# Performance work log

Hardware: AMD Instinct MI355X
Metric: run time of the kernel (lower is better)

## Reference

```python
import jax, jax.numpy as jnp
import numpy as np

N_, C_, H_, W_ = 8, 256, 64, 64
HEADS = 8
KS = 3
K2 = KS * KS
OUT = 256
HD = OUT // HEADS
STRIDE = 1
PAD = 1


def setup_inputs() -> dict:
    key = jax.random.key(0)
    ks = jax.random.split(key, 8)
    s = 0.05
    return {
        "input_features": jax.random.normal(ks[0], (N_, C_, H_, W_), jnp.float32),
        "Wq": jax.random.normal(ks[1], (OUT, C_), jnp.float32) * s,
        "Wk": jax.random.normal(ks[2], (OUT, C_), jnp.float32) * s,
        "Wv": jax.random.normal(ks[3], (OUT, C_), jnp.float32) * s,
        "off_w": jax.random.normal(ks[4], (HEADS * K2 * 2, C_, KS, KS), jnp.float32) * 0.01,
        "off_b": jnp.zeros((HEADS * K2 * 2,), jnp.float32),
        "attn_w": jax.random.normal(ks[5], (HEADS * K2, C_, KS, KS), jnp.float32) * 0.01,
        "attn_b": jnp.zeros((HEADS * K2,), jnp.float32),
        "Wo": jax.random.normal(ks[6], (OUT, OUT), jnp.float32) * s,
    }


def _conv2d(x, w, b):
    out = jax.lax.conv_general_dilated(
        x, w, (STRIDE, STRIDE), [(PAD, PAD), (PAD, PAD)],
        dimension_numbers=("NCHW", "OIHW", "NCHW"))
    return out + b[None, :, None, None]


def reference(input_features, Wq, Wk, Wv, off_w, off_b, attn_w, attn_b, Wo):
    x = input_features
    N, C, H, W = x.shape
    # query/key are projected but never used downstream in the original module
    q = jnp.einsum("oc,nchw->nohw", Wq, x)
    k = jnp.einsum("oc,nchw->nohw", Wk, x)
    v = jnp.einsum("oc,nchw->nohw", Wv, x)  # [N, OUT, H, W]

    offsets = _conv2d(x, off_w, off_b)                       # [N, HEADS*K2*2, Ho, Wo]
    aw = jax.nn.sigmoid(_conv2d(x, attn_w, attn_b))          # [N, HEADS*K2, Ho, Wo]
    Ho, Wo_sp = offsets.shape[2], offsets.shape[3]

    gx_base = jnp.linspace(-1.0, 1.0, Wo_sp)
    gy_base = jnp.linspace(-1.0, 1.0, Ho)

    # per-head, per-point (x,y) offsets, scaled by 2/[W,H] as in the source
    off = offsets.reshape(N, HEADS, K2, 2, Ho, Wo_sp)
    gx = gx_base[None, None, None, None, :] + off[:, :, :, 0] * (2.0 / W)  # [N,H,K2,Ho,Wo]
    gy = gy_base[None, None, None, :, None] + off[:, :, :, 1] * (2.0 / H)

    # grid_sample bilinear, align_corners=True, padding_mode='zeros'
    xp = (gx + 1.0) * 0.5 * (W - 1)
    yp = (gy + 1.0) * 0.5 * (H - 1)
    x0 = jnp.floor(xp).astype(jnp.int32)
    y0 = jnp.floor(yp).astype(jnp.int32)
    x1 = x0 + 1
    y1 = y0 + 1
    wx1 = xp - x0
    wx0 = 1.0 - wx1
    wy1 = yp - y0
    wy0 = 1.0 - wy1

    vf = v.reshape(N, HEADS, HD, H * W)

    def corner(yi, xi, wgt):
        valid = ((yi >= 0) & (yi < H) & (xi >= 0) & (xi < W)).astype(v.dtype)
        idx = (jnp.clip(yi, 0, H - 1) * W + jnp.clip(xi, 0, W - 1)).reshape(N, HEADS, -1)
        g = jnp.take_along_axis(vf, idx[:, :, None, :], axis=3)
        g = g.reshape(N, HEADS, HD, K2, Ho, Wo_sp)
        return g * (wgt * valid)[:, :, None]

    sampled = (corner(y0, x0, wy0 * wx0) + corner(y0, x1, wy0 * wx1)
               + corner(y1, x0, wy1 * wx0) + corner(y1, x1, wy1 * wx1))

    awr = aw.reshape(N, HEADS, K2, Ho, Wo_sp)
    head_out = jnp.einsum("nhckxy,nhkxy->nhcxy", sampled, awr)  # weighted sum over K2 points
    combined = head_out.reshape(N, OUT, Ho, Wo_sp)
    return jnp.einsum("oc,nchw->nohw", Wo, combined)
```

## Files before the change

### kernel.cpp

```cpp
#include <hip/hip_runtime.h>
#include <math.h>

#define N_    8
#define C_    256
#define H_    64
#define W_    64
#define HW    4096
#define OUT_  256
#define HEADS 8
#define HD    32
#define K2    9
#define OFFCH 144
#define AWCH  72
#define KTOT  2304
#define WPROWS 256
#define ABASE 16896

typedef __bf16 bf16x8 __attribute__((ext_vector_type(8)));
typedef __bf16 bf16x4 __attribute__((ext_vector_type(4)));
typedef float  f32x4  __attribute__((ext_vector_type(4)));

__device__ __forceinline__ void gload_lds16(const void* g, void* l) {
  __builtin_amdgcn_global_load_lds(
      (const __attribute__((address_space(1))) void*)g,
      (__attribute__((address_space(3))) void*)l, 16, 0, 0);
}

__global__ __launch_bounds__(256) void pack_x_kernel(
    const float* __restrict__ x, __bf16* __restrict__ xp)
{
  const int c0 = blockIdx.x << 6;
  const int y  = blockIdx.y;
  const int n  = blockIdx.z;
  const int tid = threadIdx.x;
  __shared__ float tile[64][65];

  const int tx = tid & 63, tg = tid >> 6;
#pragma unroll
  for (int i = 0; i < 16; ++i) {
    int cl = tg + (i << 2);
    tile[cl][tx] = x[((size_t)(n * C_ + c0 + cl) * H_ + y) * W_ + tx];
  }
  __syncthreads();
#pragma unroll
  for (int i = 0; i < 16; ++i) {
    int xl = tg + (i << 2);
    xp[((size_t)(n * HW) + y * W_ + xl) * C_ + c0 + tx] = (__bf16)tile[tx][xl];
  }
}

__global__ __launch_bounds__(256) void pack_w_kernel(
    const float* __restrict__ off_w, const float* __restrict__ off_b,
    const float* __restrict__ attn_w, const float* __restrict__ attn_b,
    __bf16* __restrict__ Wp, float* __restrict__ biasp,
    __bf16* __restrict__ zbuf)
{
  const int co = blockIdx.x;
  const int c  = threadIdx.x;
  if (co == 0) {
    *(uint4*)&zbuf[(size_t)c * 8] = make_uint4(0u, 0u, 0u, 0u);
  }
  const float* base = nullptr;
  if (co < OFFCH)      base = off_w  + ((size_t)co * C_ + c) * 9;
  else if (co < 216)   base = attn_w + ((size_t)(co - OFFCH) * C_ + c) * 9;
#pragma unroll
  for (int t = 0; t < 9; ++t) {
    float w = base ? base[t] : 0.f;
    Wp[(size_t)co * KTOT + t * C_ + c] = (__bf16)w;
  }
  if (c == 0) {
    float b = 0.f;
    if (co < OFFCH) b = off_b[co];
    else if (co < 216) b = attn_b[co - OFFCH];
    biasp[co] = b;
  }
}

__global__ __launch_bounds__(256) void pack_mat_kernel(
    const float* __restrict__ Wsrc, __bf16* __restrict__ Wdst)
{
  const int i = blockIdx.x * 256 + threadIdx.x;
  Wdst[i] = (__bf16)Wsrc[i];
}

__global__ __launch_bounds__(256) void conv_mfma_kernel(
    const __bf16* __restrict__ xp, const __bf16* __restrict__ Wp,
    const float* __restrict__ biasp, const __bf16* __restrict__ zbuf,
    __bf16* __restrict__ P2)
{
  const int yt = blockIdx.x;
  const int bn = blockIdx.y;
  const int n  = blockIdx.z;
  const int y0 = yt << 1;
  const int tid = threadIdx.x;
  const int lw = tid & 63, wv = tid >> 6;
  const int lr = lw & 15, lg = lw >> 4;

  __shared__ __align__(16) __bf16 smem[16896 + 12288];

  f32x4 acc[8][2];
#pragma unroll
  for (int m = 0; m < 8; ++m)
#pragma unroll
    for (int nt = 0; nt < 2; ++nt) acc[m][nt] = (f32x4){0.f, 0.f, 0.f, 0.f};

  if (tid < 64) {
    int p = tid & 3, cs = (tid >> 2) & 1, r = (tid >> 3) & 3, buf = tid >> 5;
    int col = cs ? 65 : 0;
    *(uint4*)&smem[((buf * 4 + r) * 66 + col) * 32 + p * 8] =
        make_uint4(0u, 0u, 0u, 0u);
  }

  int aoff[3][4];
#pragma unroll
  for (int d = 0; d < 3; ++d)
#pragma unroll
    for (int mm = 0; mm < 4; ++mm) {
      int col = (mm << 4) + lr + d;
      int p = lg ^ ((col >> 1) & 3);
      aoff[d][mm] = col * 32 + p * 8;
    }
  int boff[2];
#pragma unroll
  for (int nt = 0; nt < 2; ++nt) {
    int col = (nt << 4) + lr;
    int p = lg ^ ((col >> 1) & 3);
    boff[nt] = ABASE + wv * 3072 + col * 32 + p * 8;
  }

  const int scg = lw & 3;
  const __bf16* gB[2];
#pragma unroll
  for (int jj = 0; jj < 2; ++jj) {
    int col = (jj << 4) + (lw >> 2);
    int cg = scg ^ ((col >> 1) & 3);
    gB[jj] = Wp + (size_t)(bn * 128 + wv * 32 + col) * KTOT + (cg << 3);
  }
  const __bf16* gA[4];
  int aAdd;
  {
    int y = y0 - 1 + wv;
    bool valid = ((unsigned)y < (unsigned)H_);
    aAdd = valid ? 1 : 0;
#pragma unroll
    for (int k = 0; k < 4; ++k) {
      int col = 1 + (k << 4) + (lw >> 2);
      int cg = scg ^ ((col >> 1) & 3);
      gA[k] = valid
          ? xp + ((size_t)(n * HW) + y * W_ + (col - 1)) * C_ + (cg << 3)
          : zbuf;
    }
  }

  auto stageB = [&](int elemOff, int pbuf) {
#pragma unroll
    for (int jj = 0; jj < 2; ++jj)
      gload_lds16(gB[jj] + elemOff,
                  &smem[ABASE + wv * 3072 + pbuf * 1024 + (jj << 9)]);
  };
  auto stageA = [&](int c0elem, int buf) {
    const int add = aAdd ? c0elem : 0;
#pragma unroll
    for (int k = 0; k < 4; ++k)
      gload_lds16(gA[k] + add,
                  &smem[((buf * 4 + wv) * 66 + 1 + (k << 4)) * 32]);
  };

  stageA(0, 0);
  stageB(0 * C_ + 0, 0);
  stageB(1 * C_ + 0, 1);
  asm volatile("s_waitcnt vmcnt(4)" ::: "memory");
  __builtin_amdgcn_s_barrier();
  asm volatile("" ::: "memory");

  for (int cc = 0; cc < 4; ++cc) {
    const bool lastcc = (cc == 3);
#pragma unroll
    for (int sub = 0; sub < 2; ++sub) {
      const int ci = (cc << 1) + sub;
      const int abuf = sub;
#pragma unroll
      for (int tt = 0; tt < 9; ++tt) {
        const int dy = tt / 3, dxp = tt - dy * 3;
        const int pbR = tt % 3;
        const int pbW = (tt + 2) % 3;
        const bool lastSlice = lastcc && (sub == 1);

        if (tt == 1 && ci < 7) stageA((ci + 1) << 5, sub ^ 1);

        if (!(lastSlice && tt >= 7)) {
          const int tn  = (tt < 7) ? (tt + 2) : (tt - 7);
          const int cin = (tt < 7) ? ci : (ci + 1);
          stageB(tn * C_ + (cin << 5), pbW);
        }

        if (lastSlice && tt == 8)
          asm volatile("s_waitcnt vmcnt(0)" ::: "memory");
        else if (lastSlice && tt == 7)
          asm volatile("s_waitcnt vmcnt(2)" ::: "memory");
        else if ((tt == 1 || tt == 2) && ci < 7)
          asm volatile("s_waitcnt vmcnt(8)" ::: "memory");
        else
          asm volatile("s_waitcnt vmcnt(4)" ::: "memory");

        bf16x8 a[8], b[2];
#pragma unroll
        for (int m = 0; m < 8; ++m) {
          const int rr = (m >> 2) + dy;
          a[m] = *(const bf16x8*)&smem[aoff[dxp][m & 3] +
                                       (abuf * 4 + rr) * 2112];
        }
#pragma unroll
        for (int nt = 0; nt < 2; ++nt)
          b[nt] = *(const bf16x8*)&smem[boff[nt] + (pbR << 10)];

        __builtin_amdgcn_s_setprio(1);
#pragma unroll
        for (int m = 0; m < 8; ++m)
#pragma unroll
          for (int nt = 0; nt < 2; ++nt)
            acc[m][nt] = __builtin_amdgcn_mfma_f32_16x16x32_bf16(
                a[m], b[nt], acc[m][nt], 0, 0, 0);
        __builtin_amdgcn_s_setprio(0);

        if (tt == 8 && !lastSlice) {
          __builtin_amdgcn_s_barrier();
          asm volatile("" ::: "memory");
        }
      }
    }
  }

#pragma unroll
  for (int nt = 0; nt < 2; ++nt) {
    const int co = bn * 128 + wv * 32 + (nt << 4) + lr;
    if (co < 216) {
      const float bias = biasp[co];
      int idx;
      if (co < OFFCH) {
        int hh = co / 18;
        idx = (hh << 5) + (co - 18 * hh);
      } else {
        int r = co - OFFCH;
        int hh = r / 9;
        idx = (hh << 5) + 18 + (r - 9 * hh);
      }
#pragma unroll
      for (int m = 0; m < 8; ++m) {
#pragma unroll
        for (int reg = 0; reg < 4; ++reg) {
          const int sl = (m << 4) + (lg << 2) + reg;
          const int yout = y0 + (sl >> 6), xo = sl & 63;
          float v = acc[m][nt][reg] + bias;
          if (co >= OFFCH) v = 1.f / (1.f + expf(-v));
          P2[((size_t)n * HW + yout * W_ + xo) * 256 + idx] = (__bf16)v;
        }
      }
    }
  }
}

template <int MODE>
__global__ __launch_bounds__(256) void gemm256_kernel(
    const __bf16* __restrict__ A, const __bf16* __restrict__ Wb,
    __bf16* __restrict__ out_b, float* __restrict__ out_f)
{
  const int st = blockIdx.x;
  const int bn = blockIdx.y;
  const int n  = blockIdx.z;
  const int s0 = st << 7;
  const int tid = threadIdx.x;

  __shared__ __bf16 Asl[128][40];
  __shared__ __bf16 Bsl[128][40];

  const int lw = tid & 63, wv = tid >> 6;
  const int lr = lw & 15, lg = lw >> 4;
  const int sm_base = wv << 5;

  f32x4 acc[2][8];
#pragma unroll
  for (int m = 0; m < 2; ++m)
#pragma unroll
    for (int nt = 0; nt < 8; ++nt) acc[m][nt] = (f32x4){0.f, 0.f, 0.f, 0.f};

  for (int c0 = 0; c0 < 256; c0 += 32) {
    __syncthreads();
#pragma unroll
    for (int it = 0; it < 2; ++it) {
      int i = tid + (it << 8);
      int cg = i & 3, r = i >> 2;
      *(uint4*)&Asl[r][cg << 3] =
          *(const uint4*)&A[((size_t)n * HW + s0 + r) * 256 + c0 + (cg << 3)];
    }
#pragma unroll
    for (int it = 0; it < 2; ++it) {
      int i = tid + (it << 8);
      int cg = i & 3, r = i >> 2;
      *(uint4*)&Bsl[r][cg << 3] =
          *(const uint4*)&Wb[(size_t)((bn << 7) + r) * 256 + c0 + (cg << 3)];
    }
    __syncthreads();

    bf16x8 a0 = *(const bf16x8*)&Asl[sm_base + lr][lg << 3];
    bf16x8 a1 = *(const bf16x8*)&Asl[sm_base + 16 + lr][lg << 3];
#pragma unroll
    for (int nt = 0; nt < 8; ++nt) {
      bf16x8 b = *(const bf16x8*)&Bsl[(nt << 4) + lr][lg << 3];
      acc[0][nt] = __builtin_amdgcn_mfma_f32_16x16x32_bf16(a0, b, acc[0][nt], 0, 0, 0);
      acc[1][nt] = __builtin_amdgcn_mfma_f32_16x16x32_bf16(a1, b, acc[1][nt], 0, 0, 0);
    }
  }

#pragma unroll
  for (int m = 0; m < 2; ++m) {
#pragma unroll
    for (int nt = 0; nt < 8; ++nt) {
      const int co = (bn << 7) + (nt << 4) + lr;
      if (MODE == 0) {
#pragma unroll
        for (int reg = 0; reg < 4; ++reg) {
          const int sm = sm_base + (m << 4) + (lg << 2) + reg;
          out_b[((size_t)n * HW + s0 + sm) * 256 + co] = (__bf16)acc[m][nt][reg];
        }
      } else {
        const int sm = sm_base + (m << 4) + (lg << 2);
        float4 v4 = make_float4(acc[m][nt][0], acc[m][nt][1],
                                acc[m][nt][2], acc[m][nt][3]);
        *(float4*)&out_f[((size_t)(n * 256 + co)) * HW + s0 + sm] = v4;
      }
    }
  }
}

__global__ __launch_bounds__(256) void sample_kernel(
    const __bf16* __restrict__ vtb, const __bf16* __restrict__ P2,
    __bf16* __restrict__ comb)
{
  const int b = blockIdx.x;
  const int y = b & 63;
  const int h = (b >> 6) & 7;
  const int n = b >> 9;
  const int tid = threadIdx.x;
  const int xq = tid >> 2, cg = tid & 3;
  const int lw = tid & 63, wv = tid >> 6;

  __shared__ __align__(16) __bf16 vsl[8 * 64 * 32];

  const int xs = (wv << 4) + (lw >> 2);
  const int cs = lw & 3;
  const __bf16* vrow0 =
      vtb + ((size_t)n * HW) * 256 + (h << 5) + (cs << 3) + (size_t)xs * 256;
#pragma unroll
  for (int r = 0; r < 8; ++r) {
    int yy = y - 3 + r;
    if ((unsigned)yy < (unsigned)H_)
      gload_lds16(vrow0 + (size_t)yy * (64 * 256),
                  &vsl[(r * 64 + (wv << 4)) * 32]);
  }

  const __bf16* prow = P2 + ((size_t)n * HW + y * 64 + xq) * 256 + (h << 5);
  bf16x8 p0 = *(const bf16x8*)(prow);
  bf16x8 p1 = *(const bf16x8*)(prow + 8);
  bf16x8 p2 = *(const bf16x8*)(prow + 16);
  bf16x4 p3 = *(const bf16x4*)(prow + 24);

  __syncthreads();

  float acc[8];
#pragma unroll
  for (int j = 0; j < 8; ++j) acc[j] = 0.f;

  const __bf16* vbase = vtb + ((size_t)n * HW) * 256 + (h << 5) + (cg << 3);

#pragma unroll
  for (int k = 0; k < K2; ++k) {
    float offx, offy, a;
    if (k < 4)      { offx = (float)p0[2 * k];       offy = (float)p0[2 * k + 1]; }
    else if (k < 8) { offx = (float)p1[2 * (k - 4)]; offy = (float)p1[2 * (k - 4) + 1]; }
    else            { offx = (float)p2[0];           offy = (float)p2[1]; }
    if (k < 6)      a = (float)p2[2 + k];
    else            a = (float)p3[k - 6];

    const float xpf = (float)xq + offx * (63.f / 64.f);
    const float ypf = (float)y  + offy * (63.f / 64.f);
    const float fx0 = floorf(xpf), fy0 = floorf(ypf);
    const int x0 = (int)fx0, y0 = (int)fy0;
    const float wx1 = xpf - fx0, wx0 = 1.f - wx1;
    const float wy1 = ypf - fy0, wy0 = 1.f - wy1;

#pragma unroll
    for (int cy = 0; cy < 2; ++cy) {
      const int yi = y0 + cy;
      if ((unsigned)yi >= (unsigned)H_) continue;
      const float wy = cy ? wy1 : wy0;
      const int ridx = yi - (y - 3);
#pragma unroll
      for (int cx = 0; cx < 2; ++cx) {
        const int xi = x0 + cx;
        if ((unsigned)xi >= (unsigned)W_) continue;
        const float cw = a * wy * (cx ? wx1 : wx0);
        bf16x8 v;
        if ((unsigned)ridx < 8u) {
          v = *(const bf16x8*)&vsl[(ridx * 64 + xi) * 32 + (cg << 3)];
        } else {
          v = *(const bf16x8*)(vbase + (size_t)(yi * W_ + xi) * 256);
        }
#pragma unroll
        for (int j = 0; j < 8; ++j) acc[j] = fmaf(cw, (float)v[j], acc[j]);
      }
    }
  }

  bf16x8 r;
#pragma unroll
  for (int j = 0; j < 8; ++j) r[j] = (__bf16)acc[j];
  *(bf16x8*)&comb[((size_t)n * HW + y * 64 + xq) * 256 + (h << 5) + (cg << 3)] = r;
}

extern "C" void kernel_launch(void* const* d_in, const int* in_sizes, int n_in,
                              void* d_out, int out_size, void* d_ws,
                              size_t ws_size, hipStream_t stream)
{
  const float* x      = (const float*)d_in[0];
  const float* Wv     = (const float*)d_in[3];
  const float* off_w  = (const float*)d_in[4];
  const float* off_b  = (const float*)d_in[5];
  const float* attn_w = (const float*)d_in[6];
  const float* attn_b = (const float*)d_in[7];
  const float* Wo     = (const float*)d_in[8];
  float* out = (float*)d_out;

  __bf16* vtb   = (__bf16*)d_ws;
  __bf16* xp    = vtb + (size_t)N_ * HW * OUT_;
  __bf16* comb  = xp + (size_t)N_ * HW * C_;
  __bf16* P2    = comb + (size_t)N_ * HW * OUT_;
  __bf16* Wp    = P2 + (size_t)N_ * HW * 256;
  __bf16* Wvb   = Wp + (size_t)WPROWS * KTOT;
  __bf16* Wob   = Wvb + (size_t)OUT_ * C_;
  __bf16* zbuf  = Wob + (size_t)OUT_ * OUT_;
  float*  biasp = (float*)(zbuf + 2048);

  pack_w_kernel<<<dim3(256), 256, 0, stream>>>(off_w, off_b, attn_w, attn_b,
                                               Wp, biasp, zbuf);
  pack_mat_kernel<<<dim3(256), 256, 0, stream>>>(Wv, Wvb);
  pack_mat_kernel<<<dim3(256), 256, 0, stream>>>(Wo, Wob);
  pack_x_kernel<<<dim3(4, 64, N_), 256, 0, stream>>>(x, xp);
  conv_mfma_kernel<<<dim3(32, 2, N_), 256, 0, stream>>>(xp, Wp, biasp, zbuf, P2);
  gemm256_kernel<0><<<dim3(32, 2, N_), 256, 0, stream>>>(xp, Wvb, vtb, nullptr);
  sample_kernel<<<dim3(N_ * HEADS * H_), 256, 0, stream>>>(vtb, P2, comb);
  gemm256_kernel<1><<<dim3(32, 2, N_), 256, 0, stream>>>(comb, Wob, nullptr,
                                                         out);
}
```

Baseline: 124.4 us.

## Triple-buffer gemm256 K-loop with async global-to-LDS loads and XOR swizzle

Replaces the synchronous register-staged LDS fills in the 256-wide GEMM kernel with direct global_load_lds transfers into a three-stage ring buffer. Loads run two K-steps ahead and are gated by vmcnt waits, so memory latency overlaps with MFMA work instead of sitting behind two syncthreads per iteration. The LDS layout switches from padded rows to an XOR-swizzled unpadded layout to avoid bank conflicts, and MFMA issue priority is raised. In exchange it uses more shared memory (48KB), which can lower occupancy, and it relies on exact vmcnt accounting for correctness.

```diff
diff --git a/kernel.cpp b/kernel.cpp
--- a/kernel.cpp
+++ b/kernel.cpp
@@ -270,46 +270,86 @@
   const int n  = blockIdx.z;
   const int s0 = st << 7;
   const int tid = threadIdx.x;
-
-  __shared__ __bf16 Asl[128][40];
-  __shared__ __bf16 Bsl[128][40];
-
   const int lw = tid & 63, wv = tid >> 6;
   const int lr = lw & 15, lg = lw >> 4;
   const int sm_base = wv << 5;
 
+  __shared__ __align__(16) __bf16 smem[24576];
+
   f32x4 acc[2][8];
 #pragma unroll
   for (int m = 0; m < 2; ++m)
 #pragma unroll
     for (int nt = 0; nt < 8; ++nt) acc[m][nt] = (f32x4){0.f, 0.f, 0.f, 0.f};
 
-  for (int c0 = 0; c0 < 256; c0 += 32) {
-    __syncthreads();
-#pragma unroll
-    for (int it = 0; it < 2; ++it) {
-      int i = tid + (it << 8);
-      int cg = i & 3, r = i >> 2;
-      *(uint4*)&Asl[r][cg << 3] =
-          *(const uint4*)&A[((size_t)n * HW + s0 + r) * 256 + c0 + (cg << 3)];
-    }
-#pragma unroll
-    for (int it = 0; it < 2; ++it) {
-      int i = tid + (it << 8);
-      int cg = i & 3, r = i >> 2;
-      *(uint4*)&Bsl[r][cg << 3] =
-          *(const uint4*)&Wb[(size_t)((bn << 7) + r) * 256 + c0 + (cg << 3)];
-    }
-    __syncthreads();
-
-    bf16x8 a0 = *(const bf16x8*)&Asl[sm_base + lr][lg << 3];
-    bf16x8 a1 = *(const bf16x8*)&Asl[sm_base + 16 + lr][lg << 3];
-#pragma unroll
-    for (int nt = 0; nt < 8; ++nt) {
-      bf16x8 b = *(const bf16x8*)&Bsl[(nt << 4) + lr][lg << 3];
-      acc[0][nt] = __builtin_amdgcn_mfma_f32_16x16x32_bf16(a0, b, acc[0][nt], 0, 0, 0);
-      acc[1][nt] = __builtin_amdgcn_mfma_f32_16x16x32_bf16(a1, b, acc[1][nt], 0, 0, 0);
-    }
+  int aoff[2];
+#pragma unroll
+  for (int m = 0; m < 2; ++m) {
+    int row = sm_base + (m << 4) + lr;
+    int p = lg ^ ((row >> 1) & 3);
+    aoff[m] = row * 32 + p * 8;
+  }
+  int boff[8];
+#pragma unroll
+  for (int nt = 0; nt < 8; ++nt) {
+    int row = (nt << 4) + lr;
+    int p = lg ^ ((row >> 1) & 3);
+    boff[nt] = 12288 + row * 32 + p * 8;
+  }
+
+  const __bf16* gA[2];
+  const __bf16* gB[2];
+#pragma unroll
+  for (int jj = 0; jj < 2; ++jj) {
+    int j = wv * 2 + jj;
+    int row = (j << 4) + (lw >> 2);
+    int cg = (lw & 3) ^ ((row >> 1) & 3);
+    gA[jj] = A + ((size_t)n * HW + s0 + row) * 256 + (cg << 3);
+    gB[jj] = Wb + ((size_t)((bn << 7) + row)) * 256 + (cg << 3);
+  }
+
+  auto stage = [&](int k, int buf) {
+    const int koff = k << 5;
+#pragma unroll
+    for (int jj = 0; jj < 2; ++jj)
+      gload_lds16(gA[jj] + koff, &smem[buf * 4096 + ((wv * 2 + jj) << 9)]);
+#pragma unroll
+    for (int jj = 0; jj < 2; ++jj)
+      gload_lds16(gB[jj] + koff,
+                  &smem[12288 + buf * 4096 + ((wv * 2 + jj) << 9)]);
+  };
+
+  stage(0, 0);
+  stage(1, 1);
+
+#pragma unroll
+  for (int k = 0; k < 8; ++k) {
+    if (k < 7)
+      asm volatile("s_waitcnt vmcnt(4)" ::: "memory");
+    else
+      asm volatile("s_waitcnt vmcnt(0)" ::: "memory");
+    __builtin_amdgcn_s_barrier();
+    asm volatile("" ::: "memory");
+
+    if (k + 2 < 8) stage(k + 2, (k + 2) % 3);
+
+    const int buf = k % 3;
+    bf16x8 a[2], b[8];
+#pragma unroll
+    for (int m = 0; m < 2; ++m)
+      a[m] = *(const bf16x8*)&smem[aoff[m] + buf * 4096];
+#pragma unroll
+    for (int nt = 0; nt < 8; ++nt)
+      b[nt] = *(const bf16x8*)&smem[boff[nt] + buf * 4096];
+
+    __builtin_amdgcn_s_setprio(1);
+#pragma unroll
+    for (int m = 0; m < 2; ++m)
+#pragma unroll
+      for (int nt = 0; nt < 8; ++nt)
+        acc[m][nt] = __builtin_amdgcn_mfma_f32_16x16x32_bf16(
+            a[m], b[nt], acc[m][nt], 0, 0, 0);
+    __builtin_amdgcn_s_setprio(0);
   }
 
 #pragma unroll
```

Result: faster. 117.6 us (-5.5%).
